# Kernel optimization log

Measured on AMD Instinct MI355X. Metric: run time of the kernel, lower is better.

## Reference

```python
import jax, jax.numpy as jnp
import numpy as np

N_NODES = 50000
N_EDGES = 1_600_000
D_IN = 128
D_HID = 128
D_OUT = 128


def _linear_init(key, out_dim, in_dim, bias=True):
    k1, k2 = jax.random.split(key)
    bound = 1.0 / np.sqrt(in_dim)
    W = jax.random.uniform(k1, (out_dim, in_dim), jnp.float32, -bound, bound)
    if bias:
        b = jax.random.uniform(k2, (out_dim,), jnp.float32, -bound, bound)
        return W, b
    return W, None


def _leconv_params(key, in_dim, out_dim):
    k1, k2, k3 = jax.random.split(key, 3)
    W1, b1 = _linear_init(k1, out_dim, in_dim, bias=True)   # lin1 (applied to x_j)
    W2, _ = _linear_init(k2, out_dim, in_dim, bias=False)   # lin2 (applied to x_i)
    W3, b3 = _linear_init(k3, out_dim, in_dim, bias=True)   # lin3 (skip on x_i)
    return W1, b1, W2, W3, b3


def setup_inputs() -> dict:
    key = jax.random.key(0)
    kx, ke, kw, k_in, k_mid, k_out = jax.random.split(key, 6)
    x = jax.random.normal(kx, (N_NODES, D_IN), jnp.float32)
    edge_index = jax.random.randint(ke, (2, N_EDGES), 0, N_NODES, dtype=jnp.int32)
    edge_weight = jax.random.uniform(kw, (N_EDGES,), jnp.float32)
    iW1, ib1, iW2, iW3, ib3 = _leconv_params(k_in, D_IN, D_HID)
    mW1, mb1, mW2, mW3, mb3 = _leconv_params(k_mid, D_HID, D_HID)
    oW1, ob1, oW2, oW3, ob3 = _leconv_params(k_out, D_HID, D_OUT)
    return {
        "x": x, "edge_index": edge_index, "edge_weight": edge_weight,
        "in_W1": iW1, "in_b1": ib1, "in_W2": iW2, "in_W3": iW3, "in_b3": ib3,
        "mid_W1": mW1, "mid_b1": mb1, "mid_W2": mW2, "mid_W3": mW3, "mid_b3": mb3,
        "out_W1": oW1, "out_b1": ob1, "out_W2": oW2, "out_W3": oW3, "out_b3": ob3,
        "number_of_layers": 4,
    }


def _leconv(h, src, dst, ew, W1, b1, W2, W3, b3):
    # out_i = sum_{j->i} e_ji * ((W1 x_j + b1) - W2 x_i) + (W3 x_i + b3)
    a = h @ W1.T + b1          # [N, F_out]
    b = h @ W2.T               # [N, F_out]
    msg = ew[:, None] * (a[src] - b[dst])              # [E, F_out]
    agg = jax.ops.segment_sum(msg, dst, num_segments=h.shape[0])
    return agg + h @ W3.T + b3


def _lrelu(x):
    return jnp.where(x >= 0, x, 0.1 * x)


def reference(x, edge_index, edge_weight,
              in_W1, in_b1, in_W2, in_W3, in_b3,
              mid_W1, mid_b1, mid_W2, mid_W3, mid_b3,
              out_W1, out_b1, out_W2, out_W3, out_b3,
              number_of_layers):
    src, dst = edge_index[0], edge_index[1]
    h = _lrelu(_leconv(x, src, dst, edge_weight, in_W1, in_b1, in_W2, in_W3, in_b3))
    for _ in range(number_of_layers - 2):  # shared inner weights, as in the torch module
        h = _lrelu(_leconv(h, src, dst, edge_weight, mid_W1, mid_b1, mid_W2, mid_W3, mid_b3))
    h = _lrelu(_leconv(h, src, dst, edge_weight, out_W1, out_b1, out_W2, out_W3, out_b3))
    return jax.nn.sigmoid(h)
```

## Files before the change

kernel.cpp:

```cpp
#include <hip/hip_runtime.h>
#include <hip/hip_fp16.h>
#include <math.h>

#define D 128
#define CSH 13
#define BSH 9
#define NB_MAX 128

typedef _Float16 f16;
typedef __attribute__((ext_vector_type(8))) _Float16 f16x8;
typedef __attribute__((ext_vector_type(4))) float f32x4;
typedef __attribute__((ext_vector_type(4))) int i32x4;


__global__ __launch_bounds__(256) void binA_count(
    const int* __restrict__ dst, int* __restrict__ bucketCount, int E)
{
    __shared__ int hist[NB_MAX];
    int tid = threadIdx.x;
    if (tid < NB_MAX) hist[tid] = 0;
    __syncthreads();
    int base = blockIdx.x * 4096;
    for (int i = tid; i < 4096; i += 256) {
        int e = base + i;
        if (e < E) atomicAdd(&hist[dst[e] >> BSH], 1);
    }
    __syncthreads();
    if (tid < NB_MAX && hist[tid]) atomicAdd(&bucketCount[tid], hist[tid]);
}

__global__ void bucket_scan(
    const int* __restrict__ bucketCount, int* __restrict__ bucketBase,
    int* __restrict__ bucketCursor, int* __restrict__ row_off,
    int NBUC, int E, int N)
{
    if (threadIdx.x == 0 && blockIdx.x == 0) {
        int p = 0;
        for (int b = 0; b < NBUC; ++b) {
            bucketBase[b] = p; bucketCursor[b] = p; p += bucketCount[b];
        }
        bucketBase[NBUC] = p;
        row_off[N] = E;
    }
}

__global__ __launch_bounds__(256) void binA_scatter(
    const int* __restrict__ src, const int* __restrict__ dst,
    const float* __restrict__ ew, int* __restrict__ bucketCursor,
    int4* __restrict__ binned, int E)
{
    __shared__ int hist[NB_MAX], off[NB_MAX], cbase[NB_MAX];
    int tid = threadIdx.x;
    if (tid < NB_MAX) { hist[tid] = 0; off[tid] = 0; }
    __syncthreads();
    int base = blockIdx.x * 4096;
    for (int i = tid; i < 4096; i += 256) {
        int e = base + i;
        if (e < E) atomicAdd(&hist[dst[e] >> BSH], 1);
    }
    __syncthreads();
    if (tid < NB_MAX && hist[tid])
        cbase[tid] = atomicAdd(&bucketCursor[tid], hist[tid]);
    __syncthreads();
    for (int i = tid; i < 4096; i += 256) {
        int e = base + i;
        if (e < E) {
            int d = dst[e];
            int b = d >> BSH;
            int pos = cbase[b] + atomicAdd(&off[b], 1);
            binned[pos] = make_int4(src[e], __float_as_int(ew[e]), d, 0);
        }
    }
}

__global__ __launch_bounds__(1024) void binB_kernel(
    const int4* __restrict__ binned, const int* __restrict__ bucketBase,
    int2* __restrict__ edge_s, int* __restrict__ row_off,
    float* __restrict__ sdeg, int N, int nchunk)
{
    __shared__ int hist[4096];
    __shared__ int cur[4096];
    __shared__ float sdl[512];
    __shared__ int wsum[16];

    int b    = blockIdx.x;
    int tid  = threadIdx.x;
    int ebeg = bucketBase[b], eend = bucketBase[b + 1];
    int node0 = b << BSH;
    int nib   = min(512, N - node0);

    for (int i = tid; i < 4096; i += 1024) hist[i] = 0;
    for (int i = tid; i < 512; i += 1024) sdl[i] = 0.f;
    __syncthreads();

    for (int e = ebeg + tid; e < eend; e += 1024) {
        int4 ed = binned[e];
        int dl = ed.z - node0;
        int ch = ((unsigned)ed.x) >> CSH;
        atomicAdd(&hist[dl * nchunk + ch], 1);
        atomicAdd(&sdl[dl], __int_as_float(ed.y));
    }
    __syncthreads();

    int t4 = tid * 4;
    int h0 = hist[t4], h1 = hist[t4 + 1], h2 = hist[t4 + 2], h3 = hist[t4 + 3];
    int sum = h0 + h1 + h2 + h3;
    int lane = tid & 63, wid = tid >> 6;
    int x = sum;
    #pragma unroll
    for (int o = 1; o < 64; o <<= 1) { int t = __shfl_up(x, o); if (lane >= o) x += t; }
    if (lane == 63) wsum[wid] = x;
    __syncthreads();
    if (tid < 16) {
        int y = wsum[tid];
        #pragma unroll
        for (int o = 1; o < 16; o <<= 1) { int t = __shfl_up(y, o, 16); if (tid >= o) y += t; }
        wsum[tid] = y;
    }
    __syncthreads();
    int excl = (wid ? wsum[wid - 1] : 0) + x - sum;
    cur[t4] = excl; cur[t4 + 1] = excl + h0;
    cur[t4 + 2] = excl + h0 + h1; cur[t4 + 3] = excl + h0 + h1 + h2;
    __syncthreads();

    for (int dl = tid; dl < nib; dl += 1024) {
        row_off[node0 + dl] = ebeg + cur[dl * nchunk];
        sdeg[node0 + dl]    = sdl[dl];
    }
    __syncthreads();

    for (int e = ebeg + tid; e < eend; e += 1024) {
        int4 ed = binned[e];
        int dl = ed.z - node0;
        int ch = ((unsigned)ed.x) >> CSH;
        int pos = ebeg + atomicAdd(&cur[dl * nchunk + ch], 1);
        edge_s[pos] = make_int2(ed.x, ed.y);
    }
}

__global__ __launch_bounds__(256) void pack_kernel(
    const float* __restrict__ W1, const float* __restrict__ W2,
    const float* __restrict__ W3, f16* __restrict__ Wp)
{
    int idx = blockIdx.x * 256 + threadIdx.x;
    if (idx >= 6144) return;
    int lane = idx & 63;
    int t    = idx >> 6;
    int ks   = t & 3;
    int mot  = t >> 2;
    int m    = mot >> 3;
    int ot   = mot & 7;
    const float* W = (m == 0) ? W1 : (m == 1) ? W2 : W3;
    int o  = ot * 16 + (lane & 15);
    int kb = ks * 32 + (lane >> 4) * 8;
    f16x8 hi, lo;
    #pragma unroll
    for (int j = 0; j < 8; ++j) {
        float v = W[(size_t)o * D + kb + j];
        f16 hh = (f16)v;
        hi[j] = hh;
        lo[j] = (f16)(v - (float)hh);
    }
    size_t base = (size_t)ks * 24576 + (size_t)mot * 1024 + (size_t)lane * 8;
    *(f16x8*)&Wp[base]       = hi;
    *(f16x8*)&Wp[base + 512] = lo;
}


__global__ __launch_bounds__(256, 2) void gemm_kernel(
    const float* __restrict__ in, const f16* __restrict__ Wp,
    const float* __restrict__ b1, const float* __restrict__ b3,
    const float* __restrict__ sdeg, float* __restrict__ aA,
    float* __restrict__ aB, float* __restrict__ base_out,
    int N, int ntiles, int gridb)
{
    int tid  = threadIdx.x;
    int lane = tid & 63;
    int wid  = tid >> 6;
    int col  = lane & 15;
    int g    = lane >> 4;

    f16x8 w[3][2][4][2];
    #pragma unroll
    for (int m = 0; m < 3; ++m)
        #pragma unroll
        for (int oti = 0; oti < 2; ++oti) {
            int mot = m * 8 + wid * 2 + oti;
            #pragma unroll
            for (int ks = 0; ks < 4; ++ks) {
                const f16* p = Wp + (size_t)ks * 24576 + (size_t)mot * 1024 + (size_t)lane * 8;
                w[m][oti][ks][0] = *(const f16x8*)p;
                w[m][oti][ks][1] = *(const f16x8*)(p + 512);
            }
        }

    float bi1[2], bi3[2];
    #pragma unroll
    for (int oti = 0; oti < 2; ++oti) {
        int o = (wid * 2 + oti) * 16 + col;
        bi1[oti] = b1[o];
        bi3[oti] = b3[o];
    }

    for (int t = blockIdx.x; t < ntiles; t += gridb) {
        int n0   = t * 16;
        int nrow = n0 + col;

        f32x4 acc[3][2];
        #pragma unroll
        for (int m = 0; m < 3; ++m)
            #pragma unroll
            for (int oti = 0; oti < 2; ++oti)
                acc[m][oti] = (f32x4){0.f, 0.f, 0.f, 0.f};

        #pragma unroll
        for (int ks = 0; ks < 4; ++ks) {
            float av[8];
            if (nrow < N) {
                float4 a0 = *(const float4*)&in[(size_t)nrow * D + ks * 32 + g * 8];
                float4 a1 = *(const float4*)&in[(size_t)nrow * D + ks * 32 + g * 8 + 4];
                av[0] = a0.x; av[1] = a0.y; av[2] = a0.z; av[3] = a0.w;
                av[4] = a1.x; av[5] = a1.y; av[6] = a1.z; av[7] = a1.w;
            } else {
                #pragma unroll
                for (int j = 0; j < 8; ++j) av[j] = 0.f;
            }
            f16x8 ahi, alo;
            #pragma unroll
            for (int j = 0; j < 8; ++j) {
                f16 hh = (f16)av[j];
                ahi[j] = hh;
                alo[j] = (f16)(av[j] - (float)hh);
            }
            #pragma unroll
            for (int m = 0; m < 3; ++m)
                #pragma unroll
                for (int oti = 0; oti < 2; ++oti) {
                    acc[m][oti] = __builtin_amdgcn_mfma_f32_16x16x32_f16(ahi, w[m][oti][ks][0], acc[m][oti], 0, 0, 0);
                    acc[m][oti] = __builtin_amdgcn_mfma_f32_16x16x32_f16(alo, w[m][oti][ks][0], acc[m][oti], 0, 0, 0);
                    acc[m][oti] = __builtin_amdgcn_mfma_f32_16x16x32_f16(ahi, w[m][oti][ks][1], acc[m][oti], 0, 0, 0);
                }
        }

        float* ah = (wid < 2) ? aA : aB;
        #pragma unroll
        for (int oti = 0; oti < 2; ++oti) {
            int o  = (wid * 2 + oti) * 16 + col;
            int oh = o & 63;
            #pragma unroll
            for (int r = 0; r < 4; ++r) {
                int node = n0 + g * 4 + r;
                if (node < N) {
                    float sv   = sdeg[node];
                    float aval = acc[0][oti][r] + bi1[oti];
                    float bval = acc[2][oti][r] + bi3[oti] - sv * acc[1][oti][r];
                    ah[(size_t)node * 64 + oh]     = aval;
                    base_out[(size_t)node * D + o] = bval;
                }
            }
        }
    }
}


__global__ __launch_bounds__(256, 3) void agg_kernel(
    const float* __restrict__ aH, const float* __restrict__ base,
    const int* __restrict__ row_off, const int2* __restrict__ edge_s,
    float* __restrict__ out, int N, int hofs, int last)
{
    int lane = threadIdx.x & 63;
    int node = blockIdx.x * 4 + (threadIdx.x >> 6);
    if (node >= N) return;

    float acc = __builtin_nontemporal_load(&base[(size_t)node * D + hofs + lane]);
    int beg = row_off[node];
    int end = row_off[node + 1];

    int e = beg;
    if ((e & 1) && e < end) {
        int2 ed = edge_s[e];
        acc = fmaf(__int_as_float(ed.y), aH[(size_t)ed.x * 64 + lane], acc);
        ++e;
    }
    for (; e + 24 <= end; e += 24) {
        i32x4 ed[12];
        #pragma unroll
        for (int i = 0; i < 12; ++i)
            ed[i] = __builtin_nontemporal_load((const i32x4*)&edge_s[e + i * 2]);
        float v[24];
        #pragma unroll
        for (int i = 0; i < 12; ++i) {
            v[2 * i]     = aH[(size_t)ed[i].x * 64 + lane];
            v[2 * i + 1] = aH[(size_t)ed[i].z * 64 + lane];
        }
        #pragma unroll
        for (int i = 0; i < 12; ++i) {
            acc = fmaf(__int_as_float(ed[i].y), v[2 * i], acc);
            acc = fmaf(__int_as_float(ed[i].w), v[2 * i + 1], acc);
        }
    }
    for (; e + 8 <= end; e += 8) {
        i32x4 ed[4];
        #pragma unroll
        for (int i = 0; i < 4; ++i)
            ed[i] = __builtin_nontemporal_load((const i32x4*)&edge_s[e + i * 2]);
        float v[8];
        #pragma unroll
        for (int i = 0; i < 4; ++i) {
            v[2 * i]     = aH[(size_t)ed[i].x * 64 + lane];
            v[2 * i + 1] = aH[(size_t)ed[i].z * 64 + lane];
        }
        #pragma unroll
        for (int i = 0; i < 4; ++i) {
            acc = fmaf(__int_as_float(ed[i].y), v[2 * i], acc);
            acc = fmaf(__int_as_float(ed[i].w), v[2 * i + 1], acc);
        }
    }
    for (; e < end; ++e) {
        int2 ed = edge_s[e];
        acc = fmaf(__int_as_float(ed.y), aH[(size_t)ed.x * 64 + lane], acc);
    }

    acc = acc >= 0.f ? acc : 0.1f * acc;
    if (last) acc = 1.f / (1.f + __expf(-acc));
    __builtin_nontemporal_store(acc, &out[(size_t)node * D + hofs + lane]);
}


extern "C" void kernel_launch(void* const* d_in, const int* in_sizes, int n_in,
                              void* d_out, int out_size, void* d_ws, size_t ws_size,
                              hipStream_t stream) {
    const float* x   = (const float*)d_in[0];
    const int*   ei  = (const int*)d_in[1];
    const float* ew  = (const float*)d_in[2];
    const float* iW1 = (const float*)d_in[3];
    const float* ib1 = (const float*)d_in[4];
    const float* iW2 = (const float*)d_in[5];
    const float* iW3 = (const float*)d_in[6];
    const float* ib3 = (const float*)d_in[7];
    const float* mW1 = (const float*)d_in[8];
    const float* mb1 = (const float*)d_in[9];
    const float* mW2 = (const float*)d_in[10];
    const float* mW3 = (const float*)d_in[11];
    const float* mb3 = (const float*)d_in[12];
    const float* oW1 = (const float*)d_in[13];
    const float* ob1 = (const float*)d_in[14];
    const float* oW2 = (const float*)d_in[15];
    const float* oW3 = (const float*)d_in[16];
    const float* ob3 = (const float*)d_in[17];

    int N = in_sizes[0] / D;
    int E = in_sizes[2];
    const int* src = ei;
    const int* dst = ei + E;
    int nchunk = (N + (1 << CSH) - 1) >> CSH;
    int NBUC   = (N + (1 << BSH) - 1) >> BSH;

    char* wsp = (char*)d_ws;
    size_t off = 0;
    auto alloc = [&](size_t bytes) -> void* {
        void* p = wsp + off;
        off += (bytes + 255) & ~(size_t)255;
        return p;
    };
    float* h        = (float*)alloc((size_t)N * D * 4);
    float* base     = (float*)alloc((size_t)N * D * 4);
    float* aA       = (float*)alloc((size_t)N * 64 * 4);
    float* aB       = (float*)alloc((size_t)N * 64 * 4);
    float* sdeg     = (float*)alloc((size_t)N * 4);
    int*   row_off  = (int*)alloc((size_t)(N + 1) * 4);
    int2*  edge_s   = (int2*)alloc((size_t)E * 8);
    int*   bucketCount  = (int*)alloc((size_t)(NBUC + 1) * 4);
    int*   bucketBase   = (int*)alloc((size_t)(NBUC + 1) * 4);
    int*   bucketCursor = (int*)alloc((size_t)(NBUC + 1) * 4);
    f16*   Wp       = (f16*)alloc((size_t)3 * 98304 * 2);

    int4* binned = (int4*)h;

    hipMemsetAsync(bucketCount, 0, (size_t)(NBUC + 1) * 4, stream);

    int ablocks  = (N + 3) / 4;
    int ntiles   = (N + 15) / 16;
    int gridb    = 512;
    int abblocks = (E + 4095) / 4096;

    pack_kernel<<<24, 256, 0, stream>>>(iW1, iW2, iW3, Wp);
    pack_kernel<<<24, 256, 0, stream>>>(mW1, mW2, mW3, Wp + 98304);
    pack_kernel<<<24, 256, 0, stream>>>(oW1, oW2, oW3, Wp + 2 * 98304);

    binA_count<<<abblocks, 256, 0, stream>>>(dst, bucketCount, E);
    bucket_scan<<<1, 64, 0, stream>>>(bucketCount, bucketBase, bucketCursor,
                                      row_off, NBUC, E, N);
    binA_scatter<<<abblocks, 256, 0, stream>>>(src, dst, ew, bucketCursor,
                                               binned, E);
    binB_kernel<<<NBUC, 1024, 0, stream>>>(binned, bucketBase, edge_s,
                                           row_off, sdeg, N, nchunk);

    gemm_kernel<<<gridb, 256, 0, stream>>>(x, Wp, ib1, ib3, sdeg, aA, aB, base, N, ntiles, gridb);
    agg_kernel<<<ablocks, 256, 0, stream>>>(aA, base, row_off, edge_s, h, N, 0, 0);
    agg_kernel<<<ablocks, 256, 0, stream>>>(aB, base, row_off, edge_s, h, N, 64, 0);
    for (int l = 0; l < 2; ++l) {
        gemm_kernel<<<gridb, 256, 0, stream>>>(h, Wp + 98304, mb1, mb3, sdeg, aA, aB, base, N, ntiles, gridb);
        agg_kernel<<<ablocks, 256, 0, stream>>>(aA, base, row_off, edge_s, h, N, 0, 0);
        agg_kernel<<<ablocks, 256, 0, stream>>>(aB, base, row_off, edge_s, h, N, 64, 0);
    }
    gemm_kernel<<<gridb, 256, 0, stream>>>(h, Wp + 2 * 98304, ob1, ob3, sdeg, aA, aB, base, N, ntiles, gridb);
    agg_kernel<<<ablocks, 256, 0, stream>>>(aA, base, row_off, edge_s, (float*)d_out, N, 0, 1);
    agg_kernel<<<ablocks, 256, 0, stream>>>(aB, base, row_off, edge_s, (float*)d_out, N, 64, 1);
}
```

Baseline: 771.3 us.

## Fuse half-feature aggregation passes into one kernel handling two nodes per wave

Merges the two per-layer aggregation launches (one per 64-feature half) into a single kernel where lanes 0-31 read the aA half and lanes 32-63 the aB half, each lane accumulating two features with float2 loads. Each wave now processes two destination nodes with interleaved edge loops so more gathers are in flight. This removes the duplicate read of the edge list and row offsets per layer and halves launch count. In exchange it gives up the paired 16-byte nontemporal edge loads and the deeper 24-edge unroll, and raises per-wave divergence when the two nodes' degrees differ.

```diff
diff --git a/kernel.cpp b/kernel.cpp
--- a/kernel.cpp
+++ b/kernel.cpp
@@ -10,7 +10,6 @@
 typedef _Float16 f16;
 typedef __attribute__((ext_vector_type(8))) _Float16 f16x8;
 typedef __attribute__((ext_vector_type(4))) float f32x4;
-typedef __attribute__((ext_vector_type(4))) int i32x4;
 
 
 __global__ __launch_bounds__(256) void binA_count(
@@ -263,67 +262,99 @@
 }
 
 
-__global__ __launch_bounds__(256, 3) void agg_kernel(
-    const float* __restrict__ aH, const float* __restrict__ base,
-    const int* __restrict__ row_off, const int2* __restrict__ edge_s,
-    float* __restrict__ out, int N, int hofs, int last)
+__global__ __launch_bounds__(256) void agg_kernel(
+    const float* __restrict__ aA, const float* __restrict__ aB,
+    const float* __restrict__ base, const int* __restrict__ row_off,
+    const int2* __restrict__ edge_s, float* __restrict__ out, int N, int last)
 {
     int lane = threadIdx.x & 63;
-    int node = blockIdx.x * 4 + (threadIdx.x >> 6);
-    if (node >= N) return;
-
-    float acc = __builtin_nontemporal_load(&base[(size_t)node * D + hofs + lane]);
-    int beg = row_off[node];
-    int end = row_off[node + 1];
-
-    int e = beg;
-    if ((e & 1) && e < end) {
-        int2 ed = edge_s[e];
-        acc = fmaf(__int_as_float(ed.y), aH[(size_t)ed.x * 64 + lane], acc);
-        ++e;
-    }
-    for (; e + 24 <= end; e += 24) {
-        i32x4 ed[12];
-        #pragma unroll
-        for (int i = 0; i < 12; ++i)
-            ed[i] = __builtin_nontemporal_load((const i32x4*)&edge_s[e + i * 2]);
-        float v[24];
-        #pragma unroll
-        for (int i = 0; i < 12; ++i) {
-            v[2 * i]     = aH[(size_t)ed[i].x * 64 + lane];
-            v[2 * i + 1] = aH[(size_t)ed[i].z * 64 + lane];
-        }
-        #pragma unroll
-        for (int i = 0; i < 12; ++i) {
-            acc = fmaf(__int_as_float(ed[i].y), v[2 * i], acc);
-            acc = fmaf(__int_as_float(ed[i].w), v[2 * i + 1], acc);
-        }
-    }
-    for (; e + 8 <= end; e += 8) {
-        i32x4 ed[4];
-        #pragma unroll
-        for (int i = 0; i < 4; ++i)
-            ed[i] = __builtin_nontemporal_load((const i32x4*)&edge_s[e + i * 2]);
-        float v[8];
+    int wid  = threadIdx.x >> 6;
+    int nA   = blockIdx.x * 8 + wid * 2;
+    int nB   = nA + 1;
+    if (nA >= N) return;
+    bool hasB = (nB < N);
+
+    const float* aH = (lane < 32) ? aA : aB;
+    int fo = (lane & 31) * 2;
+    int l2 = lane * 2;
+
+    float2 accA = *(const float2*)&base[(size_t)nA * D + l2];
+    int eA = row_off[nA], endA = row_off[nA + 1];
+    float2 accB = make_float2(0.f, 0.f);
+    int eB = 0, endB = 0;
+    if (hasB) {
+        accB = *(const float2*)&base[(size_t)nB * D + l2];
+        eB = row_off[nB]; endB = row_off[nB + 1];
+    }
+
+    while (eA + 4 <= endA && eB + 4 <= endB) {
+        int2 m[8];
+        #pragma unroll
+        for (int i = 0; i < 4; ++i) m[i] = edge_s[eA + i];
+        #pragma unroll
+        for (int i = 0; i < 4; ++i) m[4 + i] = edge_s[eB + i];
+        float2 v[8];
+        #pragma unroll
+        for (int i = 0; i < 8; ++i)
+            v[i] = *(const float2*)&aH[(size_t)m[i].x * 64 + fo];
         #pragma unroll
         for (int i = 0; i < 4; ++i) {
-            v[2 * i]     = aH[(size_t)ed[i].x * 64 + lane];
-            v[2 * i + 1] = aH[(size_t)ed[i].z * 64 + lane];
+            float wgt = __int_as_float(m[i].y);
+            accA.x = fmaf(wgt, v[i].x, accA.x);
+            accA.y = fmaf(wgt, v[i].y, accA.y);
         }
         #pragma unroll
         for (int i = 0; i < 4; ++i) {
-            acc = fmaf(__int_as_float(ed[i].y), v[2 * i], acc);
-            acc = fmaf(__int_as_float(ed[i].w), v[2 * i + 1], acc);
-        }
-    }
-    for (; e < end; ++e) {
-        int2 ed = edge_s[e];
-        acc = fmaf(__int_as_float(ed.y), aH[(size_t)ed.x * 64 + lane], acc);
-    }
-
-    acc = acc >= 0.f ? acc : 0.1f * acc;
-    if (last) acc = 1.f / (1.f + __expf(-acc));
-    __builtin_nontemporal_store(acc, &out[(size_t)node * D + hofs + lane]);
+            float wgt = __int_as_float(m[4 + i].y);
+            accB.x = fmaf(wgt, v[4 + i].x, accB.x);
+            accB.y = fmaf(wgt, v[4 + i].y, accB.y);
+        }
+        eA += 4; eB += 4;
+    }
+
+    auto finish = [&](int e, int end, float2& acc) {
+        for (; e + 8 <= end; e += 8) {
+            int2 m[8];
+            #pragma unroll
+            for (int i = 0; i < 8; ++i) m[i] = edge_s[e + i];
+            float2 v[8];
+            #pragma unroll
+            for (int i = 0; i < 8; ++i)
+                v[i] = *(const float2*)&aH[(size_t)m[i].x * 64 + fo];
+            #pragma unroll
+            for (int i = 0; i < 8; ++i) {
+                float wgt = __int_as_float(m[i].y);
+                acc.x = fmaf(wgt, v[i].x, acc.x);
+                acc.y = fmaf(wgt, v[i].y, acc.y);
+            }
+        }
+        for (; e < end; ++e) {
+            int2 m = edge_s[e];
+            float2 v = *(const float2*)&aH[(size_t)m.x * 64 + fo];
+            float wgt = __int_as_float(m.y);
+            acc.x = fmaf(wgt, v.x, acc.x);
+            acc.y = fmaf(wgt, v.y, acc.y);
+        }
+    };
+    finish(eA, endA, accA);
+    if (hasB) finish(eB, endB, accB);
+
+    accA.x = accA.x >= 0.f ? accA.x : 0.1f * accA.x;
+    accA.y = accA.y >= 0.f ? accA.y : 0.1f * accA.y;
+    if (last) {
+        accA.x = 1.f / (1.f + __expf(-accA.x));
+        accA.y = 1.f / (1.f + __expf(-accA.y));
+    }
+    *(float2*)&out[(size_t)nA * D + l2] = accA;
+    if (hasB) {
+        accB.x = accB.x >= 0.f ? accB.x : 0.1f * accB.x;
+        accB.y = accB.y >= 0.f ? accB.y : 0.1f * accB.y;
+        if (last) {
+            accB.x = 1.f / (1.f + __expf(-accB.x));
+            accB.y = 1.f / (1.f + __expf(-accB.y));
+        }
+        *(float2*)&out[(size_t)nB * D + l2] = accB;
+    }
 }
 
 
@@ -379,7 +410,7 @@
 
     hipMemsetAsync(bucketCount, 0, (size_t)(NBUC + 1) * 4, stream);
 
-    int ablocks  = (N + 3) / 4;
+    int ablocks  = (N + 7) / 8;
     int ntiles   = (N + 15) / 16;
     int gridb    = 512;
     int abblocks = (E + 4095) / 4096;
@@ -397,14 +428,11 @@
                                            row_off, sdeg, N, nchunk);
 
     gemm_kernel<<<gridb, 256, 0, stream>>>(x, Wp, ib1, ib3, sdeg, aA, aB, base, N, ntiles, gridb);
-    agg_kernel<<<ablocks, 256, 0, stream>>>(aA, base, row_off, edge_s, h, N, 0, 0);
-    agg_kernel<<<ablocks, 256, 0, stream>>>(aB, base, row_off, edge_s, h, N, 64, 0);
+    agg_kernel<<<ablocks, 256, 0, stream>>>(aA, aB, base, row_off, edge_s, h, N, 0);
     for (int l = 0; l < 2; ++l) {
         gemm_kernel<<<gridb, 256, 0, stream>>>(h, Wp + 98304, mb1, mb3, sdeg, aA, aB, base, N, ntiles, gridb);
-        agg_kernel<<<ablocks, 256, 0, stream>>>(aA, base, row_off, edge_s, h, N, 0, 0);
-        agg_kernel<<<ablocks, 256, 0, stream>>>(aB, base, row_off, edge_s, h, N, 64, 0);
+        agg_kernel<<<ablocks, 256, 0, stream>>>(aA, aB, base, row_off, edge_s, h, N, 0);
     }
     gemm_kernel<<<gridb, 256, 0, stream>>>(h, Wp + 2 * 98304, ob1, ob3, sdeg, aA, aB, base, N, ntiles, gridb);
-    agg_kernel<<<ablocks, 256, 0, stream>>>(aA, base, row_off, edge_s, (float*)d_out, N, 0, 1);
-    agg_kernel<<<ablocks, 256, 0, stream>>>(aB, base, row_off, edge_s, (float*)d_out, N, 64, 1);
-}
+    agg_kernel<<<ablocks, 256, 0, stream>>>(aA, aB, base, row_off, edge_s, (float*)d_out, N, 1);
+}
```

After: 678.5 us. -12.0%, faster.

## Split gather table into eight 16-feature slices with cache-sized source chunks

Applied to the files above, without the earlier changes.

The GEMM now writes the W1 output as eight 16-column slices, each laid out contiguously per node, in place of two 64-column halves. A single persistent aggregation kernel replaces the two half-width launches. Blocks are assigned to slices by blockIdx, and each wave processes four edges in parallel across lane groups, then reduces them with shuffles. Edge sorting within each destination uses finer source chunks (CSH 11, larger shared histograms), so that the gathered rows per slice stay L2-resident. The intent is to improve gather locality, at the cost of eight passes over edge indices and more shared memory in binB.

```diff
diff --git a/kernel.cpp b/kernel.cpp
--- a/kernel.cpp
+++ b/kernel.cpp
@@ -3,14 +3,14 @@
 #include <math.h>
 
 #define D 128
-#define CSH 13
+#define CSH 11
 #define BSH 9
 #define NB_MAX 128
+#define NHMAX 13312
 
 typedef _Float16 f16;
 typedef __attribute__((ext_vector_type(8))) _Float16 f16x8;
 typedef __attribute__((ext_vector_type(4))) float f32x4;
-typedef __attribute__((ext_vector_type(4))) int i32x4;
 
 
 __global__ __launch_bounds__(256) void binA_count(
@@ -78,8 +78,8 @@
     int2* __restrict__ edge_s, int* __restrict__ row_off,
     float* __restrict__ sdeg, int N, int nchunk)
 {
-    __shared__ int hist[4096];
-    __shared__ int cur[4096];
+    __shared__ int hist[NHMAX];
+    __shared__ int cur[NHMAX];
     __shared__ float sdl[512];
     __shared__ int wsum[16];
 
@@ -89,8 +89,8 @@
     int node0 = b << BSH;
     int nib   = min(512, N - node0);
 
-    for (int i = tid; i < 4096; i += 1024) hist[i] = 0;
-    for (int i = tid; i < 512; i += 1024) sdl[i] = 0.f;
+    for (int i = tid; i < NHMAX; i += 1024) hist[i] = 0;
+    if (tid < 512) sdl[tid] = 0.f;
     __syncthreads();
 
     for (int e = ebeg + tid; e < eend; e += 1024) {
@@ -102,11 +102,13 @@
     }
     __syncthreads();
 
-    int t4 = tid * 4;
-    int h0 = hist[t4], h1 = hist[t4 + 1], h2 = hist[t4 + 2], h3 = hist[t4 + 3];
-    int sum = h0 + h1 + h2 + h3;
+    int base_i = tid * 13;
+    int v[13];
+    int tot = 0;
+    #pragma unroll
+    for (int j = 0; j < 13; ++j) { v[j] = hist[base_i + j]; tot += v[j]; }
     int lane = tid & 63, wid = tid >> 6;
-    int x = sum;
+    int x = tot;
     #pragma unroll
     for (int o = 1; o < 64; o <<= 1) { int t = __shfl_up(x, o); if (lane >= o) x += t; }
     if (lane == 63) wsum[wid] = x;
@@ -118,9 +120,9 @@
         wsum[tid] = y;
     }
     __syncthreads();
-    int excl = (wid ? wsum[wid - 1] : 0) + x - sum;
-    cur[t4] = excl; cur[t4 + 1] = excl + h0;
-    cur[t4 + 2] = excl + h0 + h1; cur[t4 + 3] = excl + h0 + h1 + h2;
+    int p = (wid ? wsum[wid - 1] : 0) + x - tot;
+    #pragma unroll
+    for (int j = 0; j < 13; ++j) { cur[base_i + j] = p; p += v[j]; }
     __syncthreads();
 
     for (int dl = tid; dl < nib; dl += 1024) {
@@ -170,9 +172,8 @@
 __global__ __launch_bounds__(256, 2) void gemm_kernel(
     const float* __restrict__ in, const f16* __restrict__ Wp,
     const float* __restrict__ b1, const float* __restrict__ b3,
-    const float* __restrict__ sdeg, float* __restrict__ aA,
-    float* __restrict__ aB, float* __restrict__ base_out,
-    int N, int ntiles, int gridb)
+    const float* __restrict__ sdeg, float* __restrict__ aS,
+    float* __restrict__ base_out, int N, int ntiles, int gridb)
 {
     int tid  = threadIdx.x;
     int lane = tid & 63;
@@ -242,11 +243,10 @@
                 }
         }
 
-        float* ah = (wid < 2) ? aA : aB;
         #pragma unroll
         for (int oti = 0; oti < 2; ++oti) {
-            int o  = (wid * 2 + oti) * 16 + col;
-            int oh = o & 63;
+            int o     = (wid * 2 + oti) * 16 + col;
+            int slice = wid * 2 + oti;
             #pragma unroll
             for (int r = 0; r < 4; ++r) {
                 int node = n0 + g * 4 + r;
@@ -254,7 +254,7 @@
                     float sv   = sdeg[node];
                     float aval = acc[0][oti][r] + bi1[oti];
                     float bval = acc[2][oti][r] + bi3[oti] - sv * acc[1][oti][r];
-                    ah[(size_t)node * 64 + oh]     = aval;
+                    aS[((size_t)slice * N + node) * 16 + col] = aval;
                     base_out[(size_t)node * D + o] = bval;
                 }
             }
@@ -263,67 +263,53 @@
 }
 
 
-__global__ __launch_bounds__(256, 3) void agg_kernel(
-    const float* __restrict__ aH, const float* __restrict__ base,
+__global__ __launch_bounds__(256) void agg_kernel(
+    const float* __restrict__ aS, const float* __restrict__ base,
     const int* __restrict__ row_off, const int2* __restrict__ edge_s,
-    float* __restrict__ out, int N, int hofs, int last)
-{
-    int lane = threadIdx.x & 63;
-    int node = blockIdx.x * 4 + (threadIdx.x >> 6);
-    if (node >= N) return;
-
-    float acc = __builtin_nontemporal_load(&base[(size_t)node * D + hofs + lane]);
-    int beg = row_off[node];
-    int end = row_off[node + 1];
-
-    int e = beg;
-    if ((e & 1) && e < end) {
-        int2 ed = edge_s[e];
-        acc = fmaf(__int_as_float(ed.y), aH[(size_t)ed.x * 64 + lane], acc);
-        ++e;
-    }
-    for (; e + 24 <= end; e += 24) {
-        i32x4 ed[12];
-        #pragma unroll
-        for (int i = 0; i < 12; ++i)
-            ed[i] = __builtin_nontemporal_load((const i32x4*)&edge_s[e + i * 2]);
-        float v[24];
-        #pragma unroll
-        for (int i = 0; i < 12; ++i) {
-            v[2 * i]     = aH[(size_t)ed[i].x * 64 + lane];
-            v[2 * i + 1] = aH[(size_t)ed[i].z * 64 + lane];
-        }
-        #pragma unroll
-        for (int i = 0; i < 12; ++i) {
-            acc = fmaf(__int_as_float(ed[i].y), v[2 * i], acc);
-            acc = fmaf(__int_as_float(ed[i].w), v[2 * i + 1], acc);
-        }
-    }
-    for (; e + 8 <= end; e += 8) {
-        i32x4 ed[4];
-        #pragma unroll
-        for (int i = 0; i < 4; ++i)
-            ed[i] = __builtin_nontemporal_load((const i32x4*)&edge_s[e + i * 2]);
-        float v[8];
-        #pragma unroll
-        for (int i = 0; i < 4; ++i) {
-            v[2 * i]     = aH[(size_t)ed[i].x * 64 + lane];
-            v[2 * i + 1] = aH[(size_t)ed[i].z * 64 + lane];
-        }
-        #pragma unroll
-        for (int i = 0; i < 4; ++i) {
-            acc = fmaf(__int_as_float(ed[i].y), v[2 * i], acc);
-            acc = fmaf(__int_as_float(ed[i].w), v[2 * i + 1], acc);
-        }
-    }
-    for (; e < end; ++e) {
-        int2 ed = edge_s[e];
-        acc = fmaf(__int_as_float(ed.y), aH[(size_t)ed.x * 64 + lane], acc);
-    }
-
-    acc = acc >= 0.f ? acc : 0.1f * acc;
-    if (last) acc = 1.f / (1.f + __expf(-acc));
-    __builtin_nontemporal_store(acc, &out[(size_t)node * D + hofs + lane]);
+    float* __restrict__ out, int N, int last, int gridb)
+{
+    int lane  = threadIdx.x & 63;
+    int wid   = threadIdx.x >> 6;
+    int slice = blockIdx.x & 7;
+    int es    = lane >> 4;
+    int f     = lane & 15;
+    const float* sb = aS + (size_t)slice * N * 16;
+    int fbase = slice * 16;
+
+    int nstride = (gridb >> 3) * 4;
+    for (int n = (blockIdx.x >> 3) * 4 + wid; n < N; n += nstride) {
+        int beg = row_off[n], end = row_off[n + 1];
+        float acc = 0.f;
+        int e = beg;
+        for (; e + 16 <= end; e += 16) {
+            long long mm[4];
+            #pragma unroll
+            for (int i = 0; i < 4; ++i)
+                mm[i] = __builtin_nontemporal_load(
+                            (const long long*)&edge_s[e + i * 4 + es]);
+            float v[4];
+            #pragma unroll
+            for (int i = 0; i < 4; ++i)
+                v[i] = sb[(size_t)(int)(mm[i] & 0xffffffff) * 16 + f];
+            #pragma unroll
+            for (int i = 0; i < 4; ++i)
+                acc = fmaf(__int_as_float((int)(mm[i] >> 32)), v[i], acc);
+        }
+        for (; e < end; e += 4) {
+            int idx = e + es;
+            int2 m = (idx < end) ? edge_s[idx] : make_int2(0, 0);
+            float v = sb[(size_t)m.x * 16 + f];
+            acc = fmaf(__int_as_float(m.y), v, acc);
+        }
+        acc += __shfl_xor(acc, 16);
+        acc += __shfl_xor(acc, 32);
+        if (es == 0) {
+            float r = acc + __builtin_nontemporal_load(&base[(size_t)n * D + fbase + f]);
+            r = r >= 0.f ? r : 0.1f * r;
+            if (last) r = 1.f / (1.f + __expf(-r));
+            __builtin_nontemporal_store(r, &out[(size_t)n * D + fbase + f]);
+        }
+    }
 }
 
 
@@ -365,8 +351,7 @@
     };
     float* h        = (float*)alloc((size_t)N * D * 4);
     float* base     = (float*)alloc((size_t)N * D * 4);
-    float* aA       = (float*)alloc((size_t)N * 64 * 4);
-    float* aB       = (float*)alloc((size_t)N * 64 * 4);
+    float* aS       = (float*)alloc((size_t)N * D * 4);
     float* sdeg     = (float*)alloc((size_t)N * 4);
     int*   row_off  = (int*)alloc((size_t)(N + 1) * 4);
     int2*  edge_s   = (int2*)alloc((size_t)E * 8);
@@ -379,7 +364,7 @@
 
     hipMemsetAsync(bucketCount, 0, (size_t)(NBUC + 1) * 4, stream);
 
-    int ablocks  = (N + 3) / 4;
+    int aggb     = 2048;
     int ntiles   = (N + 15) / 16;
     int gridb    = 512;
     int abblocks = (E + 4095) / 4096;
@@ -396,15 +381,12 @@
     binB_kernel<<<NBUC, 1024, 0, stream>>>(binned, bucketBase, edge_s,
                                            row_off, sdeg, N, nchunk);
 
-    gemm_kernel<<<gridb, 256, 0, stream>>>(x, Wp, ib1, ib3, sdeg, aA, aB, base, N, ntiles, gridb);
-    agg_kernel<<<ablocks, 256, 0, stream>>>(aA, base, row_off, edge_s, h, N, 0, 0);
-    agg_kernel<<<ablocks, 256, 0, stream>>>(aB, base, row_off, edge_s, h, N, 64, 0);
+    gemm_kernel<<<gridb, 256, 0, stream>>>(x, Wp, ib1, ib3, sdeg, aS, base, N, ntiles, gridb);
+    agg_kernel<<<aggb, 256, 0, stream>>>(aS, base, row_off, edge_s, h, N, 0, aggb);
     for (int l = 0; l < 2; ++l) {
-        gemm_kernel<<<gridb, 256, 0, stream>>>(h, Wp + 98304, mb1, mb3, sdeg, aA, aB, base, N, ntiles, gridb);
-        agg_kernel<<<ablocks, 256, 0, stream>>>(aA, base, row_off, edge_s, h, N, 0, 0);
-        agg_kernel<<<ablocks, 256, 0, stream>>>(aB, base, row_off, edge_s, h, N, 64, 0);
-    }
-    gemm_kernel<<<gridb, 256, 0, stream>>>(h, Wp + 2 * 98304, ob1, ob3, sdeg, aA, aB, base, N, ntiles, gridb);
-    agg_kernel<<<ablocks, 256, 0, stream>>>(aA, base, row_off, edge_s, (float*)d_out, N, 0, 1);
-    agg_kernel<<<ablocks, 256, 0, stream>>>(aB, base, row_off, edge_s, (float*)d_out, N, 64, 1);
-}
+        gemm_kernel<<<gridb, 256, 0, stream>>>(h, Wp + 98304, mb1, mb3, sdeg, aS, base, N, ntiles, gridb);
+        agg_kernel<<<aggb, 256, 0, stream>>>(aS, base, row_off, edge_s, h, N, 0, aggb);
+    }
+    gemm_kernel<<<gridb, 256, 0, stream>>>(h, Wp + 2 * 98304, ob1, ob3, sdeg, aS, base, N, ntiles, gridb);
+    agg_kernel<<<aggb, 256, 0, stream>>>(aS, base, row_off, edge_s, (float*)d_out, N, 1, aggb);
+}
```

Result: slower. 1.244 ms (+61.3%).
